# Kernel optimization log

Hardware: AMD Instinct MI355X
Metric: run time of the kernel (lower is better)

Reference implementation:

```python
import jax, jax.numpy as jnp
import numpy as np

N_SPEAKERS = 65536
HIDDEN = 1024
EMBED = 1024
DIM_UPDATE = 2048
LN_EPS = 1e-5


def setup_inputs() -> dict:
    key = jax.random.key(0)
    ks = jax.random.split(key, 8)
    s = 0.02
    return {
        "u_t": jax.random.normal(ks[0], (EMBED,), dtype=jnp.float32),
        "speaker_embeddings": jax.random.normal(ks[1], (N_SPEAKERS, HIDDEN), dtype=jnp.float32),
        "W_attn": jax.random.normal(ks[2], (HIDDEN, EMBED), dtype=jnp.float32) * s,
        "W1": jax.random.normal(ks[3], (DIM_UPDATE, HIDDEN + 2 * EMBED), dtype=jnp.float32) * s,
        "b1": jnp.zeros((DIM_UPDATE,), dtype=jnp.float32),
        "W2": jax.random.normal(ks[4], (HIDDEN, DIM_UPDATE), dtype=jnp.float32) * s,
        "b2": jnp.zeros((HIDDEN,), dtype=jnp.float32),
        "ln_gamma": jnp.ones((HIDDEN,), dtype=jnp.float32),
        "ln_beta": jnp.zeros((HIDDEN,), dtype=jnp.float32),
        "s_i": 12345,
    }


def reference(u_t, speaker_embeddings, W_attn, W1, b1, W2, b2, ln_gamma, ln_beta, s_i):
    # query = attention_projection(u_t): Linear(embed->hidden, bias=False) -> [HIDDEN]
    query = W_attn @ u_t
    # attention over the whole speaker memory bank: [N]
    attn_weights = jax.nn.softmax(speaker_embeddings @ query, axis=0)
    # weighted sum of bank rows: [HIDDEN]
    context = attn_weights @ speaker_embeddings
    h_s = speaker_embeddings[s_i]  # [HIDDEN]
    update_material = jnp.concatenate([u_t, h_s, context], axis=-1)  # [HIDDEN+2*EMBED]
    # update_gate: Linear -> GELU -> (dropout=id) -> Linear -> (dropout=id) -> LayerNorm
    h = jax.nn.gelu(update_material @ W1.T + b1, approximate=False)
    o = h @ W2.T + b2
    mu = jnp.mean(o)
    var = jnp.mean(jnp.square(o - mu))
    new_h_s = (o - mu) * jax.lax.rsqrt(var + LN_EPS) * ln_gamma + ln_beta
    # clone + indexed scatter write of the residual-updated row
    new_embeddings = speaker_embeddings.at[s_i].set(h_s + new_h_s)
    return new_embeddings
```

## Files before the change

kernel.cpp:

```cpp
#include <hip/hip_runtime.h>
#include <hip/hip_bf16.h>
#include <math.h>

#define NSPK  65536
#define HID   1024
#define DUP   2048
#define CAT   3072
#define LN_EPS 1e-5f

constexpr int K1_NBLK = 512;

#define WS_QUERY   0
#define WS_CONTEXT 1024
#define WS_H       2048
#define WS_O       4096
#define WS_PM      5120
#define WS_PL      5632
#define WS_PC      6144

__device__ __forceinline__ float wave_sum64(float d) {
#pragma unroll
  for (int s = 32; s > 0; s >>= 1) d += __shfl_xor(d, s, 64);
  return d;
}

__global__ __launch_bounds__(256) void k0_query(
    const float* __restrict__ W_attn, const float* __restrict__ u_t,
    float* __restrict__ query) {
  const int lane = threadIdx.x & 63;
  const int wv = threadIdx.x >> 6;
  const int row = blockIdx.x * 4 + wv;
  const float* rp = W_attn + (size_t)row * HID;
  float d = 0.f;
#pragma unroll
  for (int i = 0; i < 4; ++i) {
    float4 v = *(const float4*)(rp + i * 256 + lane * 4);
    float4 u = *(const float4*)(u_t + i * 256 + lane * 4);
    d += v.x * u.x + v.y * u.y + v.z * u.z + v.w * u.w;
  }
  d = wave_sum64(d);
  if (lane == 0) query[row] = d;
}

__global__ __launch_bounds__(256) void k1_pass(
    const float* __restrict__ emb, const float* __restrict__ query,
    float* __restrict__ out, float* __restrict__ pm, float* __restrict__ pl,
    float* __restrict__ pc) {
  const int tid = threadIdx.x;
  const int lane = tid & 63;
  const int wv = tid >> 6;
  const int gw = blockIdx.x * 4 + wv;
  const int col = lane * 4;

  float4 q0 = *(const float4*)(query + 0 * 256 + col);
  float4 q1 = *(const float4*)(query + 1 * 256 + col);
  float4 q2 = *(const float4*)(query + 2 * 256 + col);
  float4 q3 = *(const float4*)(query + 3 * 256 + col);

  float m = -INFINITY, l = 0.f;
  float4 c0 = {0.f, 0.f, 0.f, 0.f}, c1 = c0, c2 = c0, c3 = c0;

  const int row0 = gw * 32;
  for (int r = 0; r < 32; ++r) {
    const size_t base = (size_t)(row0 + r) * HID;
    const float* rp = emb + base;
    float4 v0 = *(const float4*)(rp + 0 * 256 + col);
    float4 v1 = *(const float4*)(rp + 1 * 256 + col);
    float4 v2 = *(const float4*)(rp + 2 * 256 + col);
    float4 v3 = *(const float4*)(rp + 3 * 256 + col);
    float* op = out + base;
    *(float4*)(op + 0 * 256 + col) = v0;
    *(float4*)(op + 1 * 256 + col) = v1;
    *(float4*)(op + 2 * 256 + col) = v2;
    *(float4*)(op + 3 * 256 + col) = v3;
    float d = v0.x * q0.x + v0.y * q0.y + v0.z * q0.z + v0.w * q0.w +
              v1.x * q1.x + v1.y * q1.y + v1.z * q1.z + v1.w * q1.w +
              v2.x * q2.x + v2.y * q2.y + v2.z * q2.z + v2.w * q2.w +
              v3.x * q3.x + v3.y * q3.y + v3.z * q3.z + v3.w * q3.w;
    d = wave_sum64(d);
    float mn = fmaxf(m, d);
    float alpha = __expf(m - mn);
    float w = __expf(d - mn);
    l = l * alpha + w;
    c0.x = c0.x * alpha + w * v0.x; c0.y = c0.y * alpha + w * v0.y;
    c0.z = c0.z * alpha + w * v0.z; c0.w = c0.w * alpha + w * v0.w;
    c1.x = c1.x * alpha + w * v1.x; c1.y = c1.y * alpha + w * v1.y;
    c1.z = c1.z * alpha + w * v1.z; c1.w = c1.w * alpha + w * v1.w;
    c2.x = c2.x * alpha + w * v2.x; c2.y = c2.y * alpha + w * v2.y;
    c2.z = c2.z * alpha + w * v2.z; c2.w = c2.w * alpha + w * v2.w;
    c3.x = c3.x * alpha + w * v3.x; c3.y = c3.y * alpha + w * v3.y;
    c3.z = c3.z * alpha + w * v3.z; c3.w = c3.w * alpha + w * v3.w;
    m = mn;
  }

  __shared__ float sm[4], sl[4];
  __shared__ float sc[4][HID];
  if (lane == 0) { sm[wv] = m; sl[wv] = l; }
  *(float4*)(&sc[wv][0 * 256 + col]) = c0;
  *(float4*)(&sc[wv][1 * 256 + col]) = c1;
  *(float4*)(&sc[wv][2 * 256 + col]) = c2;
  *(float4*)(&sc[wv][3 * 256 + col]) = c3;
  __syncthreads();

  float M = fmaxf(fmaxf(sm[0], sm[1]), fmaxf(sm[2], sm[3]));
  float w0 = __expf(sm[0] - M), w1 = __expf(sm[1] - M);
  float w2 = __expf(sm[2] - M), w3 = __expf(sm[3] - M);

  const int cc = tid * 4;
  float4 a;
  a.x = w0 * sc[0][cc + 0] + w1 * sc[1][cc + 0] + w2 * sc[2][cc + 0] + w3 * sc[3][cc + 0];
  a.y = w0 * sc[0][cc + 1] + w1 * sc[1][cc + 1] + w2 * sc[2][cc + 1] + w3 * sc[3][cc + 1];
  a.z = w0 * sc[0][cc + 2] + w1 * sc[1][cc + 2] + w2 * sc[2][cc + 2] + w3 * sc[3][cc + 2];
  a.w = w0 * sc[0][cc + 3] + w1 * sc[1][cc + 3] + w2 * sc[2][cc + 3] + w3 * sc[3][cc + 3];
  *(float4*)(pc + (size_t)blockIdx.x * HID + cc) = a;
  if (tid == 0) {
    pm[blockIdx.x] = M;
    pl[blockIdx.x] = w0 * sl[0] + w1 * sl[1] + w2 * sl[2] + w3 * sl[3];
  }
}

__global__ __launch_bounds__(256) void k2_reduce(
    const float* __restrict__ pm, const float* __restrict__ pl,
    const float* __restrict__ pc, float* __restrict__ context) {
  __shared__ float red[256];
  const int tid = threadIdx.x;
  const int lane = tid & 63;
  const int wv = tid >> 6;

  float mx = -INFINITY;
  for (int p = tid; p < K1_NBLK; p += 256) mx = fmaxf(mx, pm[p]);
  red[tid] = mx;
  __syncthreads();
  for (int s = 128; s > 0; s >>= 1) {
    if (tid < s) red[tid] = fmaxf(red[tid], red[tid + s]);
    __syncthreads();
  }
  const float M = red[0];
  __syncthreads();

  float ls = 0.f;
  for (int p = tid; p < K1_NBLK; p += 256) ls += __expf(pm[p] - M) * pl[p];
  red[tid] = ls;
  __syncthreads();
  for (int s = 128; s > 0; s >>= 1) {
    if (tid < s) red[tid] += red[tid + s];
    __syncthreads();
  }
  const float L = red[0];
  __syncthreads();

  const int c0 = blockIdx.x * 64;
  float acc = 0.f;
  for (int p = wv; p < K1_NBLK; p += 4) {
    float w = __expf(pm[p] - M);
    acc += w * pc[(size_t)p * HID + c0 + lane];
  }
  __shared__ float sc2[4][64];
  sc2[wv][lane] = acc;
  __syncthreads();
  if (tid < 64) {
    float s = sc2[0][tid] + sc2[1][tid] + sc2[2][tid] + sc2[3][tid];
    context[c0 + tid] = s / L;
  }
}

__global__ __launch_bounds__(256) void k3_fc1(
    const float* __restrict__ W1, const float* __restrict__ b1,
    const float* __restrict__ u_t, const float* __restrict__ emb,
    const int* __restrict__ s_i_p, const float* __restrict__ context,
    float* __restrict__ h) {
  const int lane = threadIdx.x & 63;
  const int wv = threadIdx.x >> 6;
  const int row = blockIdx.x * 4 + wv;
  const float* rp = W1 + (size_t)row * CAT;
  const int s_i = *s_i_p;
  const float* hs = emb + (size_t)s_i * HID;
  float d = 0.f;
#pragma unroll
  for (int i = 0; i < 12; ++i) {
    const int k = i * 256 + lane * 4;
    float4 v = *(const float4*)(rp + k);
    const float* src = (i < 4) ? (u_t + k) : (i < 8) ? (hs + k - 1024)
                                                     : (context + k - 2048);
    float4 u = *(const float4*)src;
    d += v.x * u.x + v.y * u.y + v.z * u.z + v.w * u.w;
  }
  d = wave_sum64(d);
  if (lane == 0) {
    float x = d + b1[row];
    h[row] = 0.5f * x * (1.0f + erff(x * 0.70710678118654752f));
  }
}

__global__ __launch_bounds__(256) void k4_fc2(
    const float* __restrict__ W2, const float* __restrict__ b2,
    const float* __restrict__ h, float* __restrict__ o) {
  const int lane = threadIdx.x & 63;
  const int wv = threadIdx.x >> 6;
  const int row = blockIdx.x * 4 + wv;
  const float* rp = W2 + (size_t)row * DUP;
  float d = 0.f;
#pragma unroll
  for (int i = 0; i < 8; ++i) {
    const int k = i * 256 + lane * 4;
    float4 v = *(const float4*)(rp + k);
    float4 u = *(const float4*)(h + k);
    d += v.x * u.x + v.y * u.y + v.z * u.z + v.w * u.w;
  }
  d = wave_sum64(d);
  if (lane == 0) o[row] = d + b2[row];
}

__global__ __launch_bounds__(256) void k5_ln_scatter(
    const float* __restrict__ o, const float* __restrict__ gamma,
    const float* __restrict__ beta, const float* __restrict__ emb,
    const int* __restrict__ s_i_p, float* __restrict__ out) {
  __shared__ float red[256];
  const int tid = threadIdx.x;
  float4 v = *(const float4*)(o + tid * 4);
  float s = v.x + v.y + v.z + v.w;
  red[tid] = s;
  __syncthreads();
  for (int t = 128; t > 0; t >>= 1) {
    if (tid < t) red[tid] += red[tid + t];
    __syncthreads();
  }
  const float mu = red[0] * (1.0f / HID);
  __syncthreads();
  float dx = v.x - mu, dy = v.y - mu, dz = v.z - mu, dw = v.w - mu;
  red[tid] = dx * dx + dy * dy + dz * dz + dw * dw;
  __syncthreads();
  for (int t = 128; t > 0; t >>= 1) {
    if (tid < t) red[tid] += red[tid + t];
    __syncthreads();
  }
  const float var = red[0] * (1.0f / HID);
  const float inv = rsqrtf(var + LN_EPS);
  const int s_i = *s_i_p;
  const float* hs = emb + (size_t)s_i * HID;
  float4 g = *(const float4*)(gamma + tid * 4);
  float4 b = *(const float4*)(beta + tid * 4);
  float4 hv = *(const float4*)(hs + tid * 4);
  float4 r;
  r.x = hv.x + dx * inv * g.x + b.x;
  r.y = hv.y + dy * inv * g.y + b.y;
  r.z = hv.z + dz * inv * g.z + b.z;
  r.w = hv.w + dw * inv * g.w + b.w;
  *(float4*)(out + (size_t)s_i * HID + tid * 4) = r;
}

extern "C" void kernel_launch(void* const* d_in, const int* in_sizes, int n_in,
                              void* d_out, int out_size, void* d_ws, size_t ws_size,
                              hipStream_t stream) {
  const float* u_t     = (const float*)d_in[0];
  const float* emb     = (const float*)d_in[1];
  const float* W_attn  = (const float*)d_in[2];
  const float* W1      = (const float*)d_in[3];
  const float* b1      = (const float*)d_in[4];
  const float* W2      = (const float*)d_in[5];
  const float* b2      = (const float*)d_in[6];
  const float* gamma   = (const float*)d_in[7];
  const float* beta    = (const float*)d_in[8];
  const int*   s_i_p   = (const int*)d_in[9];
  float* out = (float*)d_out;

  float* ws = (float*)d_ws;
  float* query   = ws + WS_QUERY;
  float* context = ws + WS_CONTEXT;
  float* h       = ws + WS_H;
  float* o       = ws + WS_O;
  float* pm      = ws + WS_PM;
  float* pl      = ws + WS_PL;
  float* pc      = ws + WS_PC;

  k0_query<<<256, 256, 0, stream>>>(W_attn, u_t, query);
  k1_pass<<<K1_NBLK, 256, 0, stream>>>(emb, query, out, pm, pl, pc);
  k2_reduce<<<16, 256, 0, stream>>>(pm, pl, pc, context);
  k3_fc1<<<512, 256, 0, stream>>>(W1, b1, u_t, emb, s_i_p, context, h);
  k4_fc2<<<256, 256, 0, stream>>>(W2, b2, h, o);
  k5_ln_scatter<<<1, 256, 0, stream>>>(o, gamma, beta, emb, s_i_p, out);
}
```

Before: 532.7 us.

## Double-buffer bank streaming with nontemporal I/O, lazy softmax rescale, wider reduce

The main streaming pass now uses nontemporal loads and stores, prefetches the next row into registers, and halves the rows per wave while doubling the block count. Online softmax rescaling only happens when the running max rises by more than a threshold, which removes most per-row exp and multiply work. The partial reduction kernel is spread over more blocks and caches the per-block weights in shared memory. Vector ext types replace float4 across all kernels. The lazy rescale allows the unnormalised sums to grow by up to exp(8), which could affect precision, and the extra partials add traffic to the reduction.

```diff
diff --git a/kernel.cpp b/kernel.cpp
--- a/kernel.cpp
+++ b/kernel.cpp
@@ -1,5 +1,4 @@
 #include <hip/hip_runtime.h>
-#include <hip/hip_bf16.h>
 #include <math.h>
 
 #define NSPK  65536
@@ -8,15 +7,18 @@
 #define CAT   3072
 #define LN_EPS 1e-5f
 
-constexpr int K1_NBLK = 512;
+typedef float f4 __attribute__((ext_vector_type(4)));
+
+constexpr int K1_NBLK = 1024;
+constexpr int K2_NBLK = 64;
 
 #define WS_QUERY   0
 #define WS_CONTEXT 1024
 #define WS_H       2048
 #define WS_O       4096
 #define WS_PM      5120
-#define WS_PL      5632
-#define WS_PC      6144
+#define WS_PL      (WS_PM + K1_NBLK)
+#define WS_PC      8192
 
 __device__ __forceinline__ float wave_sum64(float d) {
 #pragma unroll
@@ -34,9 +36,10 @@
   float d = 0.f;
 #pragma unroll
   for (int i = 0; i < 4; ++i) {
-    float4 v = *(const float4*)(rp + i * 256 + lane * 4);
-    float4 u = *(const float4*)(u_t + i * 256 + lane * 4);
-    d += v.x * u.x + v.y * u.y + v.z * u.z + v.w * u.w;
+    f4 v = *(const f4*)(rp + i * 256 + lane * 4);
+    f4 u = *(const f4*)(u_t + i * 256 + lane * 4);
+    f4 p = v * u;
+    d += p.x + p.y + p.z + p.w;
   }
   d = wave_sum64(d);
   if (lane == 0) query[row] = d;
@@ -52,67 +55,67 @@
   const int gw = blockIdx.x * 4 + wv;
   const int col = lane * 4;
 
-  float4 q0 = *(const float4*)(query + 0 * 256 + col);
-  float4 q1 = *(const float4*)(query + 1 * 256 + col);
-  float4 q2 = *(const float4*)(query + 2 * 256 + col);
-  float4 q3 = *(const float4*)(query + 3 * 256 + col);
+  f4 q0 = *(const f4*)(query + 0 * 256 + col);
+  f4 q1 = *(const f4*)(query + 1 * 256 + col);
+  f4 q2 = *(const f4*)(query + 2 * 256 + col);
+  f4 q3 = *(const f4*)(query + 3 * 256 + col);
 
   float m = -INFINITY, l = 0.f;
-  float4 c0 = {0.f, 0.f, 0.f, 0.f}, c1 = c0, c2 = c0, c3 = c0;
-
-  const int row0 = gw * 32;
-  for (int r = 0; r < 32; ++r) {
-    const size_t base = (size_t)(row0 + r) * HID;
-    const float* rp = emb + base;
-    float4 v0 = *(const float4*)(rp + 0 * 256 + col);
-    float4 v1 = *(const float4*)(rp + 1 * 256 + col);
-    float4 v2 = *(const float4*)(rp + 2 * 256 + col);
-    float4 v3 = *(const float4*)(rp + 3 * 256 + col);
-    float* op = out + base;
-    *(float4*)(op + 0 * 256 + col) = v0;
-    *(float4*)(op + 1 * 256 + col) = v1;
-    *(float4*)(op + 2 * 256 + col) = v2;
-    *(float4*)(op + 3 * 256 + col) = v3;
-    float d = v0.x * q0.x + v0.y * q0.y + v0.z * q0.z + v0.w * q0.w +
-              v1.x * q1.x + v1.y * q1.y + v1.z * q1.z + v1.w * q1.w +
-              v2.x * q2.x + v2.y * q2.y + v2.z * q2.z + v2.w * q2.w +
-              v3.x * q3.x + v3.y * q3.y + v3.z * q3.z + v3.w * q3.w;
+  f4 c0 = {0.f, 0.f, 0.f, 0.f}, c1 = c0, c2 = c0, c3 = c0;
+
+  const int row0 = gw * 16;
+  const float* rp0 = emb + (size_t)row0 * HID + col;
+  f4 v0 = __builtin_nontemporal_load((const f4*)(rp0 + 0 * 256));
+  f4 v1 = __builtin_nontemporal_load((const f4*)(rp0 + 1 * 256));
+  f4 v2 = __builtin_nontemporal_load((const f4*)(rp0 + 2 * 256));
+  f4 v3 = __builtin_nontemporal_load((const f4*)(rp0 + 3 * 256));
+
+  for (int r = 0; r < 16; ++r) {
+    f4 n0, n1, n2, n3;
+    if (r < 15) {
+      const float* np = emb + (size_t)(row0 + r + 1) * HID + col;
+      n0 = __builtin_nontemporal_load((const f4*)(np + 0 * 256));
+      n1 = __builtin_nontemporal_load((const f4*)(np + 1 * 256));
+      n2 = __builtin_nontemporal_load((const f4*)(np + 2 * 256));
+      n3 = __builtin_nontemporal_load((const f4*)(np + 3 * 256));
+    } else {
+      n0 = v0; n1 = v1; n2 = v2; n3 = v3;
+    }
+    float* op = out + (size_t)(row0 + r) * HID + col;
+    __builtin_nontemporal_store(v0, (f4*)(op + 0 * 256));
+    __builtin_nontemporal_store(v1, (f4*)(op + 1 * 256));
+    __builtin_nontemporal_store(v2, (f4*)(op + 2 * 256));
+    __builtin_nontemporal_store(v3, (f4*)(op + 3 * 256));
+    f4 p = v0 * q0 + v1 * q1 + v2 * q2 + v3 * q3;
+    float d = p.x + p.y + p.z + p.w;
     d = wave_sum64(d);
-    float mn = fmaxf(m, d);
-    float alpha = __expf(m - mn);
-    float w = __expf(d - mn);
-    l = l * alpha + w;
-    c0.x = c0.x * alpha + w * v0.x; c0.y = c0.y * alpha + w * v0.y;
-    c0.z = c0.z * alpha + w * v0.z; c0.w = c0.w * alpha + w * v0.w;
-    c1.x = c1.x * alpha + w * v1.x; c1.y = c1.y * alpha + w * v1.y;
-    c1.z = c1.z * alpha + w * v1.z; c1.w = c1.w * alpha + w * v1.w;
-    c2.x = c2.x * alpha + w * v2.x; c2.y = c2.y * alpha + w * v2.y;
-    c2.z = c2.z * alpha + w * v2.z; c2.w = c2.w * alpha + w * v2.w;
-    c3.x = c3.x * alpha + w * v3.x; c3.y = c3.y * alpha + w * v3.y;
-    c3.z = c3.z * alpha + w * v3.z; c3.w = c3.w * alpha + w * v3.w;
-    m = mn;
+    if (d > m + 8.f) {
+      float alpha = __expf(m - d);
+      l *= alpha;
+      c0 *= alpha; c1 *= alpha; c2 *= alpha; c3 *= alpha;
+      m = d;
+    }
+    float w = __expf(d - m);
+    l += w;
+    c0 += w * v0; c1 += w * v1; c2 += w * v2; c3 += w * v3;
+    v0 = n0; v1 = n1; v2 = n2; v3 = n3;
   }
 
   __shared__ float sm[4], sl[4];
-  __shared__ float sc[4][HID];
+  __shared__ f4 sc[4][256];
   if (lane == 0) { sm[wv] = m; sl[wv] = l; }
-  *(float4*)(&sc[wv][0 * 256 + col]) = c0;
-  *(float4*)(&sc[wv][1 * 256 + col]) = c1;
-  *(float4*)(&sc[wv][2 * 256 + col]) = c2;
-  *(float4*)(&sc[wv][3 * 256 + col]) = c3;
-  __syncthreads();
-
-  float M = fmaxf(fmaxf(sm[0], sm[1]), fmaxf(sm[2], sm[3]));
-  float w0 = __expf(sm[0] - M), w1 = __expf(sm[1] - M);
-  float w2 = __expf(sm[2] - M), w3 = __expf(sm[3] - M);
-
-  const int cc = tid * 4;
-  float4 a;
-  a.x = w0 * sc[0][cc + 0] + w1 * sc[1][cc + 0] + w2 * sc[2][cc + 0] + w3 * sc[3][cc + 0];
-  a.y = w0 * sc[0][cc + 1] + w1 * sc[1][cc + 1] + w2 * sc[2][cc + 1] + w3 * sc[3][cc + 1];
-  a.z = w0 * sc[0][cc + 2] + w1 * sc[1][cc + 2] + w2 * sc[2][cc + 2] + w3 * sc[3][cc + 2];
-  a.w = w0 * sc[0][cc + 3] + w1 * sc[1][cc + 3] + w2 * sc[2][cc + 3] + w3 * sc[3][cc + 3];
-  *(float4*)(pc + (size_t)blockIdx.x * HID + cc) = a;
+  sc[wv][0 * 64 + lane] = c0;
+  sc[wv][1 * 64 + lane] = c1;
+  sc[wv][2 * 64 + lane] = c2;
+  sc[wv][3 * 64 + lane] = c3;
+  __syncthreads();
+
+  const float M = fmaxf(fmaxf(sm[0], sm[1]), fmaxf(sm[2], sm[3]));
+  const float w0 = __expf(sm[0] - M), w1 = __expf(sm[1] - M);
+  const float w2 = __expf(sm[2] - M), w3 = __expf(sm[3] - M);
+
+  f4 a = w0 * sc[0][tid] + w1 * sc[1][tid] + w2 * sc[2][tid] + w3 * sc[3][tid];
+  ((f4*)(pc + (size_t)blockIdx.x * HID))[tid] = a;
   if (tid == 0) {
     pm[blockIdx.x] = M;
     pl[blockIdx.x] = w0 * sl[0] + w1 * sl[1] + w2 * sl[2] + w3 * sl[3];
@@ -123,9 +126,8 @@
     const float* __restrict__ pm, const float* __restrict__ pl,
     const float* __restrict__ pc, float* __restrict__ context) {
   __shared__ float red[256];
+  __shared__ float sw[K1_NBLK];
   const int tid = threadIdx.x;
-  const int lane = tid & 63;
-  const int wv = tid >> 6;
 
   float mx = -INFINITY;
   for (int p = tid; p < K1_NBLK; p += 256) mx = fmaxf(mx, pm[p]);
@@ -139,29 +141,35 @@
   __syncthreads();
 
   float ls = 0.f;
-  for (int p = tid; p < K1_NBLK; p += 256) ls += __expf(pm[p] - M) * pl[p];
+  for (int p = tid; p < K1_NBLK; p += 256) {
+    float w = __expf(pm[p] - M);
+    sw[p] = w;
+    ls += w * pl[p];
+  }
   red[tid] = ls;
   __syncthreads();
   for (int s = 128; s > 0; s >>= 1) {
     if (tid < s) red[tid] += red[tid + s];
     __syncthreads();
   }
-  const float L = red[0];
-  __syncthreads();
-
-  const int c0 = blockIdx.x * 64;
+  const float invL = 1.f / red[0];
+
+  const int ci = tid & 15;
+  const int p0 = tid >> 4;
+  const int c = blockIdx.x * 16 + ci;
   float acc = 0.f;
-  for (int p = wv; p < K1_NBLK; p += 4) {
-    float w = __expf(pm[p] - M);
-    acc += w * pc[(size_t)p * HID + c0 + lane];
-  }
-  __shared__ float sc2[4][64];
-  sc2[wv][lane] = acc;
-  __syncthreads();
-  if (tid < 64) {
-    float s = sc2[0][tid] + sc2[1][tid] + sc2[2][tid] + sc2[3][tid];
-    context[c0 + tid] = s / L;
-  }
+#pragma unroll 4
+  for (int p = p0; p < K1_NBLK; p += 16)
+    acc += sw[p] * pc[(size_t)p * HID + c];
+
+  __shared__ float sacc[256];
+  sacc[tid] = acc;
+  __syncthreads();
+  for (int s = 128; s >= 16; s >>= 1) {
+    if (tid < s) sacc[tid] += sacc[tid + s];
+    __syncthreads();
+  }
+  if (tid < 16) context[blockIdx.x * 16 + tid] = sacc[tid] * invL;
 }
 
 __global__ __launch_bounds__(256) void k3_fc1(
@@ -179,11 +187,12 @@
 #pragma unroll
   for (int i = 0; i < 12; ++i) {
     const int k = i * 256 + lane * 4;
-    float4 v = *(const float4*)(rp + k);
+    f4 v = *(const f4*)(rp + k);
     const float* src = (i < 4) ? (u_t + k) : (i < 8) ? (hs + k - 1024)
                                                      : (context + k - 2048);
-    float4 u = *(const float4*)src;
-    d += v.x * u.x + v.y * u.y + v.z * u.z + v.w * u.w;
+    f4 u = *(const f4*)src;
+    f4 p = v * u;
+    d += p.x + p.y + p.z + p.w;
   }
   d = wave_sum64(d);
   if (lane == 0) {
@@ -203,9 +212,10 @@
 #pragma unroll
   for (int i = 0; i < 8; ++i) {
     const int k = i * 256 + lane * 4;
-    float4 v = *(const float4*)(rp + k);
-    float4 u = *(const float4*)(h + k);
-    d += v.x * u.x + v.y * u.y + v.z * u.z + v.w * u.w;
+    f4 v = *(const f4*)(rp + k);
+    f4 u = *(const f4*)(h + k);
+    f4 p = v * u;
+    d += p.x + p.y + p.z + p.w;
   }
   d = wave_sum64(d);
   if (lane == 0) o[row] = d + b2[row];
@@ -217,7 +227,7 @@
     const int* __restrict__ s_i_p, float* __restrict__ out) {
   __shared__ float red[256];
   const int tid = threadIdx.x;
-  float4 v = *(const float4*)(o + tid * 4);
+  f4 v = *(const f4*)(o + tid * 4);
   float s = v.x + v.y + v.z + v.w;
   red[tid] = s;
   __syncthreads();
@@ -238,15 +248,15 @@
   const float inv = rsqrtf(var + LN_EPS);
   const int s_i = *s_i_p;
   const float* hs = emb + (size_t)s_i * HID;
-  float4 g = *(const float4*)(gamma + tid * 4);
-  float4 b = *(const float4*)(beta + tid * 4);
-  float4 hv = *(const float4*)(hs + tid * 4);
-  float4 r;
+  f4 g = *(const f4*)(gamma + tid * 4);
+  f4 b = *(const f4*)(beta + tid * 4);
+  f4 hv = *(const f4*)(hs + tid * 4);
+  f4 r;
   r.x = hv.x + dx * inv * g.x + b.x;
   r.y = hv.y + dy * inv * g.y + b.y;
   r.z = hv.z + dz * inv * g.z + b.z;
   r.w = hv.w + dw * inv * g.w + b.w;
-  *(float4*)(out + (size_t)s_i * HID + tid * 4) = r;
+  *(f4*)(out + (size_t)s_i * HID + tid * 4) = r;
 }
 
 extern "C" void kernel_launch(void* const* d_in, const int* in_sizes, int n_in,
@@ -275,7 +285,7 @@
 
   k0_query<<<256, 256, 0, stream>>>(W_attn, u_t, query);
   k1_pass<<<K1_NBLK, 256, 0, stream>>>(emb, query, out, pm, pl, pc);
-  k2_reduce<<<16, 256, 0, stream>>>(pm, pl, pc, context);
+  k2_reduce<<<K2_NBLK, 256, 0, stream>>>(pm, pl, pc, context);
   k3_fc1<<<512, 256, 0, stream>>>(W1, b1, u_t, emb, s_i_p, context, h);
   k4_fc2<<<256, 256, 0, stream>>>(W2, b2, h, o);
   k5_ln_scatter<<<1, 256, 0, stream>>>(o, gamma, beta, emb, s_i_p, out);
```

Result: faster. 495.2 us (-7.0%).
